# Kernel optimization log

Hardware: AMD Instinct MI355X
Metric: run time of the kernel (lower is better)

Reference implementation:

```python
import jax, jax.numpy as jnp
from jax import lax
import numpy as np

T, B, DIM_F, DIM_H, DIM_S, DIM_W = 1024, 32, 512, 512, 1024, 512


def setup_inputs() -> dict:
    key = jax.random.key(0)
    ks = jax.random.split(key, 9)
    F_matrix = jax.random.normal(ks[0], (T, DIM_F), dtype=jnp.float32)
    a_prev = jax.nn.softmax(jax.random.normal(ks[1], (B, T), dtype=jnp.float32), axis=1)
    s_prev = jax.random.normal(ks[2], (B, DIM_S), dtype=jnp.float32)
    h = jax.random.normal(ks[3], (T, B, DIM_H), dtype=jnp.float32)
    # Linear weights stored as [in, out] so y = x @ W (+ b)
    Ww = jax.random.normal(ks[4], (DIM_S, DIM_W), dtype=jnp.float32) / np.sqrt(DIM_S)
    Vw = jax.random.normal(ks[5], (DIM_H, DIM_W), dtype=jnp.float32) / np.sqrt(DIM_H)
    Vb = jax.random.normal(ks[6], (DIM_W,), dtype=jnp.float32) * 0.01
    Uw = jax.random.normal(ks[7], (DIM_F, DIM_W), dtype=jnp.float32) / np.sqrt(DIM_F)
    ww = jax.random.normal(ks[8], (DIM_W,), dtype=jnp.float32) / np.sqrt(DIM_W)
    return {"F_matrix": F_matrix, "a_prev": a_prev, "s_prev": s_prev, "h": h,
            "Ww": Ww, "Vw": Vw, "Vb": Vb, "Uw": Uw, "ww": ww, "beta": 1}


def _calc_f(F_matrix, a_prev):
    # torch.conv2d(input=[1,1,T,dim_f], weight=[B,1,T,1], padding=[(T-1)//2, 0])
    t = F_matrix.shape[0]
    pad = (t - 1) // 2
    lhs = F_matrix[None, None]          # [1, 1, T, dim_f]
    rhs = a_prev[:, None, :, None]      # [B, 1, T, 1]
    f = lax.conv_general_dilated(
        lhs, rhs, window_strides=(1, 1), padding=[(pad, pad), (0, 0)],
        dimension_numbers=("NCHW", "OIHW", "NCHW"))[0]  # [B, T_out, dim_f]
    if f.shape[1] != t:  # even T -> T_out = T-1; pad one leading time row with zeros
        f = jnp.pad(f, ((0, 0), (1, 0), (0, 0)))
    return f


def reference(F_matrix, a_prev, s_prev, h, Ww, Vw, Vb, Uw, ww, beta):
    f_current = _calc_f(F_matrix, a_prev)                 # [B, T, dim_f]
    hT = jnp.swapaxes(h, 0, 1)                            # [B, T, dim_h]
    x = jnp.tanh(jnp.matmul(s_prev, Ww)[:, None, :]       # Ws: [B, 1, dim_w]
                 + jnp.matmul(hT, Vw) + Vb                # Vh: [B, T, dim_w]
                 + jnp.matmul(f_current, Uw))             # Uf: [B, T, dim_w]
    e_current = jnp.einsum("btw,w->bt", x, ww)            # [B, T]
    return jax.nn.softmax(beta * e_current, axis=1)       # 'sharpening' mode
```

## Files before the change

kernel.cpp:

```cpp
#include <hip/hip_runtime.h>
#include <hip/hip_bf16.h>
#include <math.h>

#define T_DIM 1024
#define B_DIM 32
#define DIMF 512
#define DIMH 512
#define DIMS 1024
#define DIMW 512

typedef __attribute__((ext_vector_type(8))) short short8;
typedef __attribute__((ext_vector_type(4))) float f32x4;

__device__ __forceinline__ unsigned f2bf1(float x) {
    unsigned a = __float_as_uint(x);
    return (a + 0x7FFFu + ((a >> 16) & 1u)) >> 16;
}
__device__ __forceinline__ unsigned f2bf2(float lo, float hi) {
    return f2bf1(lo) | (f2bf1(hi) << 16);
}
__device__ __forceinline__ float fast_tanh(float x) {
    return 1.f - __fdividef(2.f, 1.f + __expf(x + x));
}
__device__ __forceinline__ unsigned short bf1(float x) {
    __hip_bfloat16 b = __float2bfloat16(x);
    return *reinterpret_cast<unsigned short*>(&b);
}
__device__ __forceinline__ short8 pack8(float4 a, float4 c) {
    union { unsigned short us[8]; short8 s; } u;
    u.us[0] = bf1(a.x); u.us[1] = bf1(a.y); u.us[2] = bf1(a.z); u.us[3] = bf1(a.w);
    u.us[4] = bf1(c.x); u.us[5] = bf1(c.y); u.us[6] = bf1(c.z); u.us[7] = bf1(c.w);
    return u.s;
}

__device__ __forceinline__ void gl16(const unsigned short* g, unsigned short* l) {
    __builtin_amdgcn_global_load_lds(
        (const __attribute__((address_space(1))) unsigned int*)g,
        (__attribute__((address_space(3))) unsigned int*)l, 16, 0, 0);
}
__device__ __forceinline__ void gl16f(const float* g, float* l) {
    __builtin_amdgcn_global_load_lds(
        (const __attribute__((address_space(1))) unsigned int*)g,
        (__attribute__((address_space(3))) unsigned int*)l, 16, 0, 0);
}

__global__ void __launch_bounds__(256) k_prep_all(
    const float* __restrict__ F, const float* __restrict__ Uw,
    const float* __restrict__ Vw, const float* __restrict__ a_prev,
    const float* __restrict__ s_prev, const float* __restrict__ Ww,
    const float* __restrict__ Vb, const float* __restrict__ h,
    unsigned short* __restrict__ GT, unsigned short* __restrict__ VwT,
    unsigned short* __restrict__ P, float* __restrict__ SWp,
    unsigned short* __restrict__ hB, int nPack) {
    __shared__ float sh[8192];
    const int bz = blockIdx.x;
    const int tid = threadIdx.x;

    if (bz < nPack) {
        for (unsigned i = bz * 256 + tid; i < 32768u * 64; i += (unsigned)nPack * 256) {
            const int r = i >> 6, c8 = (i & 63) * 8;
            const int bb = r >> 10, t = r & 1023;
            const float* src = h + ((size_t)(t * 32 + bb)) * 512 + c8;
            const float4 v0 = *(const float4*)(src);
            const float4 v1 = *(const float4*)(src + 4);
            union { unsigned short us[8]; uint4 u4; } o;
            o.us[0] = bf1(v0.x); o.us[1] = bf1(v0.y);
            o.us[2] = bf1(v0.z); o.us[3] = bf1(v0.w);
            o.us[4] = bf1(v1.x); o.us[5] = bf1(v1.y);
            o.us[6] = bf1(v1.z); o.us[7] = bf1(v1.w);
            *(uint4*)(hB + (size_t)r * 512 + c8) = o.u4;
        }
        return;
    }
    const int bz2 = bz - nPack;
    if (bz2 < 512) {
        const int rt = bz2 & 63, ct = bz2 >> 6;
        const int r0g = rt * 16;
        const float4* Fv = (const float4*)(F + (size_t)r0g * DIMF);
        float4* shv = (float4*)sh;
        for (int i = tid; i < 16 * DIMF / 4; i += 256) shv[i] = Fv[i];
        __syncthreads();
        const int c = ct * 64 + (tid & 63);
        const int r0 = (tid >> 6) * 4;
        float acc[4] = {0.f, 0.f, 0.f, 0.f};
        for (int k = 0; k < DIMF; ++k) {
            const float bv = Uw[(size_t)k * DIMW + c];
#pragma unroll
            for (int j = 0; j < 4; ++j)
                acc[j] = fmaf(sh[(r0 + j) * DIMF + k], bv, acc[j]);
        }
        uint2 o;
        o.x = f2bf2(acc[0], acc[1]);
        o.y = f2bf2(acc[2], acc[3]);
        *(uint2*)(GT + (size_t)c * T_DIM + r0g + r0) = o;
        return;
    }
    const int bz3 = bz2 - 512;
    if (bz3 < 512) {
        if (bz3 < 256) {
            const int k0 = (bz3 >> 4) * 32, n0 = (bz3 & 15) * 32;
            const int x = tid & 31, y = tid >> 5;
#pragma unroll
            for (int i = 0; i < 4; ++i)
                sh[(y + 8 * i) * 33 + x] = Vw[(size_t)(k0 + y + 8 * i) * DIMW + n0 + x];
            __syncthreads();
#pragma unroll
            for (int i = 0; i < 4; ++i) {
                const int n = n0 + y + 8 * i;
                VwT[(size_t)n * DIMH + k0 + x] = (unsigned short)f2bf1(sh[x * 33 + y + 8 * i]);
            }
        } else {
            const int bs = bz3 - 256;
            const int b = bs >> 3, s = bs & 7;
            for (int i = tid; i < 2048; i += 256) {
                const int j = i + s;
                float v = 0.f;
                if (j >= 512 && j < 1536) v = a_prev[(size_t)b * T_DIM + j - 512];
                P[(size_t)bs * 2048 + i] = (unsigned short)f2bf1(v);
            }
        }
        return;
    }
    {
        const int bz4 = bz3 - 512;
        const int c0 = (bz4 & 15) * 32, q = bz4 >> 4;
        float (*shb)[256] = (float(*)[256])sh;
        for (int i = tid; i < 32 * 64; i += 256) {
            const int r = i >> 6, c4 = (i & 63) * 4;
            *(float4*)&shb[r][c4] = *(const float4*)(s_prev + (size_t)r * DIMS + q * 256 + c4);
        }
        __syncthreads();
        const int c  = c0 + (tid & 31);
        const int bg = tid >> 5;
        float acc[4];
#pragma unroll
        for (int j = 0; j < 4; ++j) acc[j] = (q == 0) ? Vb[c] : 0.f;
        const float* W = Ww + (size_t)q * 256 * DIMW;
        for (int k = 0; k < 256; ++k) {
            const float w = W[(size_t)k * DIMW + c];
#pragma unroll
            for (int j = 0; j < 4; ++j)
                acc[j] = fmaf(shb[bg + 8 * j][k], w, acc[j]);
        }
#pragma unroll
        for (int j = 0; j < 4; ++j)
            SWp[((size_t)q * B_DIM + bg + 8 * j) * DIMW + c] = acc[j];
    }
}

template <bool PACKED>
__global__ void __launch_bounds__(256, 3) k_main(
    const float* __restrict__ hF, const unsigned short* __restrict__ hB,
    const unsigned short* __restrict__ VwT, const unsigned short* __restrict__ GT,
    const unsigned short* __restrict__ P, const float* __restrict__ SWp,
    const float* __restrict__ ww, float* __restrict__ ep) {
    __shared__ __align__(16) float AsF[PACKED ? 4096 : 8192];
    __shared__ unsigned short Bs[128 * 64];
    unsigned short* As2 = (unsigned short*)AsF;

    const int bid = blockIdx.x;
    const int wg  = (bid & 7) * 128 + (bid >> 3);
    const int x = wg & 3, yy = wg >> 2;
    const int w0 = x * 128;
    const int b  = yy >> 3;
    const int t0 = (yy & 7) * 128;

    const int tid  = threadIdx.x;
    const int lane = tid & 63;
    const int wv   = tid >> 6;
    const int wm = wv >> 1, wn = wv & 1;
    const int g = lane >> 4, r16 = lane & 15;
    const int s7 = r16 & 7;

    f32x4 acc[4][4];
#pragma unroll
    for (int m = 0; m < 4; ++m)
#pragma unroll
        for (int n = 0; n < 4; ++n) acc[m][n] = (f32x4)0.f;

    const int kstart = max(0, t0 - 512);
    const int kend   = min(T_DIM - 1, t0 + 639);
    const int NS2    = (kend - kstart + 1) >> 6;

    const int rB = lane >> 3;
    const int cB = ((lane & 7) ^ rB) * 8;
    const unsigned short* hSb[4];
#pragma unroll
    for (int q = 0; q < 4; ++q)
        hSb[q] = hB + ((size_t)(b * 1024 + t0 + wv * 32 + q * 8 + rB)) * 512 + cB;
    const float* hS[8];
    {
        const int rl = lane >> 4, cl = lane & 15;
#pragma unroll
        for (int q = 0; q < 8; ++q) {
            const int row = wv * 32 + q * 4 + rl;
            hS[q] = hF + ((size_t)(t0 + row) * B_DIM + b) * DIMH + ((cl ^ (row & 7)) << 2);
        }
    }
    const unsigned short* vS[4];
    const unsigned short* gS[4];
#pragma unroll
    for (int q = 0; q < 4; ++q) {
        vS[q] = VwT + (size_t)(w0 + wv * 32 + q * 8 + rB) * DIMH + cB;
        gS[q] = GT  + (size_t)(w0 + wv * 32 + q * 8 + rB) * T_DIM + kstart + cB;
    }
    const unsigned short* Pb = P + (size_t)b * 8 * 2048;
    const unsigned short* pS[4];
#pragma unroll
    for (int q = 0; q < 4; ++q) {
        const int row = wv * 32 + q * 8 + rB;
        const int jb = kstart + ((lane & 7) ^ rB) * 8 + 1024 - (t0 + row);
        const int sj = jb & 7;
        pS[q] = Pb + sj * 2048 + (jb - sj);
    }
    const bool zrow = (t0 + wm * 64 + r16 == 0);

    for (int k0 = 0; k0 < DIMH; k0 += 64) {
        __syncthreads();
        if (PACKED) {
#pragma unroll
            for (int q = 0; q < 4; ++q) gl16(hSb[q] + k0, As2 + (wv * 32 + q * 8) * 64);
        } else {
#pragma unroll
            for (int q = 0; q < 8; ++q) gl16f(hS[q] + k0, AsF + (wv * 32 + q * 4) * 64);
        }
#pragma unroll
        for (int q = 0; q < 4; ++q) gl16(vS[q] + k0, Bs + (wv * 32 + q * 8) * 64);
        __syncthreads();

#pragma unroll
        for (int ks = 0; ks < 2; ++ks) {
            short8 af[4], bf[4];
            if (PACKED) {
#pragma unroll
                for (int m = 0; m < 4; ++m)
                    af[m] = *(const short8*)&As2[(wm * 64 + m * 16 + r16) * 64 +
                                                 ((ks * 4 + g) ^ s7) * 8];
            } else {
#pragma unroll
                for (int m = 0; m < 4; ++m) {
                    const int base = (wm * 64 + m * 16 + r16) * 64;
                    const int clo = ((ks * 8 + 2 * g) ^ s7) * 4;
                    const int chi = ((ks * 8 + 2 * g + 1) ^ s7) * 4;
                    af[m] = pack8(*(const float4*)&AsF[base + clo],
                                  *(const float4*)&AsF[base + chi]);
                }
            }
#pragma unroll
            for (int n = 0; n < 4; ++n)
                bf[n] = *(const short8*)&Bs[(wn * 64 + n * 16 + r16) * 64 +
                                            ((ks * 4 + g) ^ s7) * 8];
#pragma unroll
            for (int m = 0; m < 4; ++m)
#pragma unroll
                for (int n = 0; n < 4; ++n)
                    acc[m][n] = __builtin_amdgcn_mfma_f32_16x16x32_bf16(
                        af[m], bf[n], acc[m][n], 0, 0, 0);
        }
    }

    for (int s2 = 0; s2 < NS2; ++s2) {
        const int o = s2 * 64;
        __syncthreads();
#pragma unroll
        for (int q = 0; q < 4; ++q) gl16(pS[q] + o, As2 + (wv * 32 + q * 8) * 64);
#pragma unroll
        for (int q = 0; q < 4; ++q) gl16(gS[q] + o, Bs + (wv * 32 + q * 8) * 64);
        __syncthreads();

#pragma unroll
        for (int ks = 0; ks < 2; ++ks) {
            short8 af[4], bf[4];
#pragma unroll
            for (int m = 0; m < 4; ++m)
                af[m] = *(const short8*)&As2[(wm * 64 + m * 16 + r16) * 64 +
                                             ((ks * 4 + g) ^ s7) * 8];
            if (zrow) af[0] = (short8)(short)0;
#pragma unroll
            for (int n = 0; n < 4; ++n)
                bf[n] = *(const short8*)&Bs[(wn * 64 + n * 16 + r16) * 64 +
                                            ((ks * 4 + g) ^ s7) * 8];
#pragma unroll
            for (int m = 0; m < 4; ++m)
#pragma unroll
                for (int n = 0; n < 4; ++n)
                    acc[m][n] = __builtin_amdgcn_mfma_f32_16x16x32_bf16(
                        af[m], bf[n], acc[m][n], 0, 0, 0);
        }
    }

    float swv[4], wwv[4];
#pragma unroll
    for (int n = 0; n < 4; ++n) {
        const int w = w0 + wn * 64 + n * 16 + r16;
        float sv = 0.f;
#pragma unroll
        for (int q = 0; q < 4; ++q)
            sv += SWp[((size_t)q * B_DIM + b) * DIMW + w];
        swv[n] = sv;
        wwv[n] = ww[w];
    }
#pragma unroll
    for (int m = 0; m < 4; ++m) {
#pragma unroll
        for (int reg = 0; reg < 4; ++reg) {
            float s = 0.f;
#pragma unroll
            for (int n = 0; n < 4; ++n)
                s = fmaf(fast_tanh(acc[m][n][reg] + swv[n]), wwv[n], s);
            s += __shfl_xor(s, 1, 64);
            s += __shfl_xor(s, 2, 64);
            s += __shfl_xor(s, 4, 64);
            s += __shfl_xor(s, 8, 64);
            if (r16 == 0) {
                const int trow = t0 + wm * 64 + m * 16 + g * 4 + reg;
                ep[((size_t)(x * 2 + wn) * B_DIM + b) * T_DIM + trow] = s;
            }
        }
    }
}

__device__ __forceinline__ float decode_beta(const void* p) {
    const int iv = *(const int*)p;
    const float fv = __int_as_float(iv);
    const float afv = fabsf(fv);
    if (afv >= 1e-6f && afv <= 1e6f) return fv;
    return (float)iv;
}

__global__ void k_softmax(const float* __restrict__ ep, const void* __restrict__ beta_p,
                          float* __restrict__ out) {
    const int b = blockIdx.x;
    const float beta = decode_beta(beta_p);
    __shared__ float redm[4];
    __shared__ float reds[4];
    float v[4];
    float m = -INFINITY;
#pragma unroll
    for (int i = 0; i < 4; ++i) {
        const int t = threadIdx.x * 4 + i;
        float ev = 0.f;
#pragma unroll
        for (int xq = 0; xq < 8; ++xq)
            ev += ep[((size_t)xq * B_DIM + b) * T_DIM + t];
        v[i] = beta * ev;
        m = fmaxf(m, v[i]);
    }
    for (int off = 1; off < 64; off <<= 1) m = fmaxf(m, __shfl_xor(m, off, 64));
    const int wid = threadIdx.x >> 6, lane = threadIdx.x & 63;
    if (lane == 0) redm[wid] = m;
    __syncthreads();
    m = fmaxf(fmaxf(redm[0], redm[1]), fmaxf(redm[2], redm[3]));
    float s = 0.f;
    float ex[4];
#pragma unroll
    for (int i = 0; i < 4; ++i) { ex[i] = expf(v[i] - m); s += ex[i]; }
    for (int off = 1; off < 64; off <<= 1) s += __shfl_xor(s, off, 64);
    if (lane == 0) reds[wid] = s;
    __syncthreads();
    s = reds[0] + reds[1] + reds[2] + reds[3];
    const float inv = 1.f / s;
#pragma unroll
    for (int i = 0; i < 4; ++i)
        out[(size_t)b * T_DIM + threadIdx.x * 4 + i] = ex[i] * inv;
}

extern "C" void kernel_launch(void* const* d_in, const int* in_sizes, int n_in,
                              void* d_out, int out_size, void* d_ws, size_t ws_size,
                              hipStream_t stream) {
    const float* F      = (const float*)d_in[0];
    const float* a_prev = (const float*)d_in[1];
    const float* s_prev = (const float*)d_in[2];
    const float* h      = (const float*)d_in[3];
    const float* Ww     = (const float*)d_in[4];
    const float* Vw     = (const float*)d_in[5];
    const float* Vb     = (const float*)d_in[6];
    const float* Uw     = (const float*)d_in[7];
    const float* ww     = (const float*)d_in[8];
    const void*  beta_p = d_in[9];
    float* out = (float*)d_out;

    char* ws = (char*)d_ws;
    unsigned short* GT  = (unsigned short*)(ws);
    unsigned short* VwT = (unsigned short*)(ws + (1u << 20));
    unsigned short* P   = (unsigned short*)(ws + (1u << 20) + (512u << 10));
    float* SWp = (float*)(ws + (2u << 20) + (512u << 10));
    float* ep  = (float*)(ws + (2u << 20) + (768u << 10));
    unsigned short* hB = (unsigned short*)(ws + (4u << 20));

    const bool big = ws_size >= (36ull << 20);
    const int nPack = big ? 1024 : 0;

    k_prep_all<<<dim3(nPack + 1088), 256, 0, stream>>>(
        F, Uw, Vw, a_prev, s_prev, Ww, Vb, h, GT, VwT, P, SWp, hB, nPack);
    if (big) {
        k_main<true><<<dim3(1024), 256, 0, stream>>>(h, hB, VwT, GT, P, SWp, ww, ep);
    } else {
        k_main<false><<<dim3(1024), 256, 0, stream>>>(h, hB, VwT, GT, P, SWp, ww, ep);
    }
    k_softmax<<<dim3(32), 256, 0, stream>>>(ep, beta_p, out);
}
```

Before: 111.2 us.

## Software-pipeline main GEMM with triple-buffered B tiles and direct A register loads

Replaces the packed main kernel with a pipelined version in which the B operand (VwT, then GT) is staged into a three-deep LDS ring two steps ahead. The A operand (bf16 h, then P) is loaded straight from global memory into registers one step ahead, with explicit vmcnt waits and a single barrier per step. This is meant to overlap global loads with MFMA work and remove the double __syncthreads per k-step. The cost is higher register pressure, since the occupancy hint of 3 is dropped, and the A loads are uncoalesced 16-byte per-lane global reads.

```diff
diff --git a/kernel.cpp b/kernel.cpp
--- a/kernel.cpp
+++ b/kernel.cpp
@@ -148,15 +148,12 @@
     }
 }
 
-template <bool PACKED>
-__global__ void __launch_bounds__(256, 3) k_main(
-    const float* __restrict__ hF, const unsigned short* __restrict__ hB,
-    const unsigned short* __restrict__ VwT, const unsigned short* __restrict__ GT,
-    const unsigned short* __restrict__ P, const float* __restrict__ SWp,
-    const float* __restrict__ ww, float* __restrict__ ep) {
-    __shared__ __align__(16) float AsF[PACKED ? 4096 : 8192];
-    __shared__ unsigned short Bs[128 * 64];
-    unsigned short* As2 = (unsigned short*)AsF;
+__global__ void __launch_bounds__(256) k_main_pipe(
+    const unsigned short* __restrict__ hB, const unsigned short* __restrict__ VwT,
+    const unsigned short* __restrict__ GT, const unsigned short* __restrict__ P,
+    const float* __restrict__ SWp, const float* __restrict__ ww,
+    float* __restrict__ ep) {
+    __shared__ unsigned short Bs[3][128 * 64];
 
     const int bid = blockIdx.x;
     const int wg  = (bid & 7) * 128 + (bid >> 3);
@@ -169,7 +166,7 @@
     const int lane = tid & 63;
     const int wv   = tid >> 6;
     const int wm = wv >> 1, wn = wv & 1;
-    const int g = lane >> 4, r16 = lane & 15;
+    const int g = lane >> 4, r16 = lane & 15, g8 = g * 8;
     const int s7 = r16 & 7;
 
     f32x4 acc[4][4];
@@ -181,13 +178,186 @@
     const int kstart = max(0, t0 - 512);
     const int kend   = min(T_DIM - 1, t0 + 639);
     const int NS2    = (kend - kstart + 1) >> 6;
+    const int NT     = 8 + NS2;
 
     const int rB = lane >> 3;
     const int cB = ((lane & 7) ^ rB) * 8;
-    const unsigned short* hSb[4];
-#pragma unroll
-    for (int q = 0; q < 4; ++q)
-        hSb[q] = hB + ((size_t)(b * 1024 + t0 + wv * 32 + q * 8 + rB)) * 512 + cB;
+    const unsigned short* vS[4];
+    const unsigned short* gS[4];
+#pragma unroll
+    for (int q = 0; q < 4; ++q) {
+        vS[q] = VwT + (size_t)(w0 + wv * 32 + q * 8 + rB) * DIMH + cB;
+        gS[q] = GT  + (size_t)(w0 + wv * 32 + q * 8 + rB) * T_DIM + kstart + cB;
+    }
+
+    const int trow0 = t0 + wm * 64 + r16;
+    const unsigned short* hA[4];
+#pragma unroll
+    for (int m = 0; m < 4; ++m)
+        hA[m] = hB + ((size_t)(b * 1024 + trow0 + m * 16)) * 512 + g8;
+    const unsigned short* Pb = P + (size_t)b * 8 * 2048;
+    const unsigned short* pA[4];
+#pragma unroll
+    for (int m = 0; m < 4; ++m) {
+        const int trow = trow0 + m * 16;
+        const int jb = kstart + g8 + 1024 - trow;
+        const int sj = jb & 7;
+        pA[m] = Pb + sj * 2048 + (jb - sj);
+    }
+    const bool zrow = (trow0 == 0);
+
+#define FENCE() __builtin_amdgcn_sched_barrier(0)
+#define STAGEB(u2, j)                                                        \
+    {                                                                        \
+        if ((u2) < 8) {                                                      \
+            _Pragma("unroll")                                                \
+            for (int q = 0; q < 4; ++q)                                      \
+                gl16(vS[q] + (u2) * 64, &Bs[j][(wv * 32 + q * 8) * 64]);     \
+        } else {                                                             \
+            _Pragma("unroll")                                                \
+            for (int q = 0; q < 4; ++q)                                      \
+                gl16(gS[q] + ((u2) - 8) * 64, &Bs[j][(wv * 32 + q * 8) * 64]); \
+        }                                                                    \
+    }
+#define LOADA(AF, u1)                                                        \
+    {                                                                        \
+        if ((u1) < 8) {                                                      \
+            _Pragma("unroll")                                                \
+            for (int m = 0; m < 4; ++m) {                                    \
+                AF[m * 2]     = *(const short8*)(hA[m] + (u1) * 64);         \
+                AF[m * 2 + 1] = *(const short8*)(hA[m] + (u1) * 64 + 32);    \
+            }                                                                \
+        } else {                                                             \
+            _Pragma("unroll")                                                \
+            for (int m = 0; m < 4; ++m) {                                    \
+                AF[m * 2]     = *(const short8*)(pA[m] + ((u1) - 8) * 64);   \
+                AF[m * 2 + 1] = *(const short8*)(pA[m] + ((u1) - 8) * 64 + 32); \
+            }                                                                \
+            if (zrow) { AF[0] = (short8)(short)0; AF[1] = (short8)(short)0; } \
+        }                                                                    \
+    }
+#define STEP(AFc, AFn, u)                                                    \
+    {                                                                        \
+        int rc2 = rc + 2; if (rc2 >= 3) rc2 -= 3;                            \
+        if ((u) + 2 < NT) STAGEB((u) + 2, rc2);                              \
+        FENCE();                                                             \
+        if ((u) + 1 < NT) LOADA(AFn, (u) + 1);                               \
+        FENCE();                                                             \
+        const unsigned short* Bc = &Bs[rc][0];                               \
+        short8 bf0[4], bf1[4];                                               \
+        _Pragma("unroll")                                                    \
+        for (int n = 0; n < 4; ++n) {                                        \
+            const int rowb = (wn * 64 + n * 16 + r16) * 64;                  \
+            bf0[n] = *(const short8*)(Bc + rowb + ((g) ^ s7) * 8);           \
+            bf1[n] = *(const short8*)(Bc + rowb + ((4 + g) ^ s7) * 8);       \
+        }                                                                    \
+        _Pragma("unroll")                                                    \
+        for (int m = 0; m < 4; ++m)                                          \
+            _Pragma("unroll")                                                \
+            for (int n = 0; n < 4; ++n)                                      \
+                acc[m][n] = __builtin_amdgcn_mfma_f32_16x16x32_bf16(         \
+                    AFc[m * 2], bf0[n], acc[m][n], 0, 0, 0);                 \
+        _Pragma("unroll")                                                    \
+        for (int m = 0; m < 4; ++m)                                          \
+            _Pragma("unroll")                                                \
+            for (int n = 0; n < 4; ++n)                                      \
+                acc[m][n] = __builtin_amdgcn_mfma_f32_16x16x32_bf16(         \
+                    AFc[m * 2 + 1], bf1[n], acc[m][n], 0, 0, 0);             \
+        FENCE();                                                             \
+        asm volatile("s_waitcnt vmcnt(12)" ::: "memory");                    \
+        __builtin_amdgcn_s_barrier();                                        \
+        FENCE();                                                             \
+        rc = rc + 1; if (rc >= 3) rc -= 3;                                   \
+    }
+
+    short8 afP[8], afQ[8];
+    STAGEB(0, 0);
+    FENCE();
+    STAGEB(1, 1);
+    FENCE();
+    LOADA(afP, 0);
+    FENCE();
+    asm volatile("s_waitcnt vmcnt(12)" ::: "memory");
+    __builtin_amdgcn_s_barrier();
+    FENCE();
+
+    int rc = 0;
+    for (int u = 0; u < NT; u += 2) {
+        STEP(afP, afQ, u);
+        STEP(afQ, afP, u + 1);
+    }
+
+#undef STAGEB
+#undef LOADA
+#undef STEP
+#undef FENCE
+
+    float swv[4], wwv[4];
+#pragma unroll
+    for (int n = 0; n < 4; ++n) {
+        const int w = w0 + wn * 64 + n * 16 + r16;
+        float sv = 0.f;
+#pragma unroll
+        for (int q = 0; q < 4; ++q)
+            sv += SWp[((size_t)q * B_DIM + b) * DIMW + w];
+        swv[n] = sv;
+        wwv[n] = ww[w];
+    }
+#pragma unroll
+    for (int m = 0; m < 4; ++m) {
+#pragma unroll
+        for (int reg = 0; reg < 4; ++reg) {
+            float s = 0.f;
+#pragma unroll
+            for (int n = 0; n < 4; ++n)
+                s = fmaf(fast_tanh(acc[m][n][reg] + swv[n]), wwv[n], s);
+            s += __shfl_xor(s, 1, 64);
+            s += __shfl_xor(s, 2, 64);
+            s += __shfl_xor(s, 4, 64);
+            s += __shfl_xor(s, 8, 64);
+            if (r16 == 0) {
+                const int trow = t0 + wm * 64 + m * 16 + g * 4 + reg;
+                ep[((size_t)(x * 2 + wn) * B_DIM + b) * T_DIM + trow] = s;
+            }
+        }
+    }
+}
+
+__global__ void __launch_bounds__(256, 3) k_main_fb(
+    const float* __restrict__ hF, const unsigned short* __restrict__ VwT,
+    const unsigned short* __restrict__ GT, const unsigned short* __restrict__ P,
+    const float* __restrict__ SWp, const float* __restrict__ ww,
+    float* __restrict__ ep) {
+    __shared__ __align__(16) float AsF[8192];
+    __shared__ unsigned short Bs[128 * 64];
+    unsigned short* As2 = (unsigned short*)AsF;
+
+    const int bid = blockIdx.x;
+    const int wg  = (bid & 7) * 128 + (bid >> 3);
+    const int x = wg & 3, yy = wg >> 2;
+    const int w0 = x * 128;
+    const int b  = yy >> 3;
+    const int t0 = (yy & 7) * 128;
+
+    const int tid  = threadIdx.x;
+    const int lane = tid & 63;
+    const int wv   = tid >> 6;
+    const int wm = wv >> 1, wn = wv & 1;
+    const int g = lane >> 4, r16 = lane & 15;
+    const int s7 = r16 & 7;
+
+    f32x4 acc[4][4];
+#pragma unroll
+    for (int m = 0; m < 4; ++m)
+#pragma unroll
+        for (int n = 0; n < 4; ++n) acc[m][n] = (f32x4)0.f;
+
+    const int kstart = max(0, t0 - 512);
+    const int kend   = min(T_DIM - 1, t0 + 639);
+    const int NS2    = (kend - kstart + 1) >> 6;
+
+    const int rB = lane >> 3;
+    const int cB = ((lane & 7) ^ rB) * 8;
     const float* hS[8];
     {
         const int rl = lane >> 4, cl = lane & 15;
@@ -217,34 +387,21 @@
 
     for (int k0 = 0; k0 < DIMH; k0 += 64) {
         __syncthreads();
-        if (PACKED) {
-#pragma unroll
-            for (int q = 0; q < 4; ++q) gl16(hSb[q] + k0, As2 + (wv * 32 + q * 8) * 64);
-        } else {
-#pragma unroll
-            for (int q = 0; q < 8; ++q) gl16f(hS[q] + k0, AsF + (wv * 32 + q * 4) * 64);
-        }
+#pragma unroll
+        for (int q = 0; q < 8; ++q) gl16f(hS[q] + k0, AsF + (wv * 32 + q * 4) * 64);
 #pragma unroll
         for (int q = 0; q < 4; ++q) gl16(vS[q] + k0, Bs + (wv * 32 + q * 8) * 64);
         __syncthreads();
-
 #pragma unroll
         for (int ks = 0; ks < 2; ++ks) {
             short8 af[4], bf[4];
-            if (PACKED) {
-#pragma unroll
-                for (int m = 0; m < 4; ++m)
-                    af[m] = *(const short8*)&As2[(wm * 64 + m * 16 + r16) * 64 +
-                                                 ((ks * 4 + g) ^ s7) * 8];
-            } else {
-#pragma unroll
-                for (int m = 0; m < 4; ++m) {
-                    const int base = (wm * 64 + m * 16 + r16) * 64;
-                    const int clo = ((ks * 8 + 2 * g) ^ s7) * 4;
-                    const int chi = ((ks * 8 + 2 * g + 1) ^ s7) * 4;
-                    af[m] = pack8(*(const float4*)&AsF[base + clo],
-                                  *(const float4*)&AsF[base + chi]);
-                }
+#pragma unroll
+            for (int m = 0; m < 4; ++m) {
+                const int base = (wm * 64 + m * 16 + r16) * 64;
+                const int clo = ((ks * 8 + 2 * g) ^ s7) * 4;
+                const int chi = ((ks * 8 + 2 * g + 1) ^ s7) * 4;
+                af[m] = pack8(*(const float4*)&AsF[base + clo],
+                              *(const float4*)&AsF[base + chi]);
             }
 #pragma unroll
             for (int n = 0; n < 4; ++n)
@@ -258,7 +415,6 @@
                         af[m], bf[n], acc[m][n], 0, 0, 0);
         }
     }
-
     for (int s2 = 0; s2 < NS2; ++s2) {
         const int o = s2 * 64;
         __syncthreads();
@@ -267,7 +423,6 @@
 #pragma unroll
         for (int q = 0; q < 4; ++q) gl16(gS[q] + o, Bs + (wv * 32 + q * 8) * 64);
         __syncthreads();
-
 #pragma unroll
         for (int ks = 0; ks < 2; ++ks) {
             short8 af[4], bf[4];
@@ -288,7 +443,6 @@
                         af[m], bf[n], acc[m][n], 0, 0, 0);
         }
     }
-
     float swv[4], wwv[4];
 #pragma unroll
     for (int n = 0; n < 4; ++n) {
@@ -394,9 +548,9 @@
     k_prep_all<<<dim3(nPack + 1088), 256, 0, stream>>>(
         F, Uw, Vw, a_prev, s_prev, Ww, Vb, h, GT, VwT, P, SWp, hB, nPack);
     if (big) {
-        k_main<true><<<dim3(1024), 256, 0, stream>>>(h, hB, VwT, GT, P, SWp, ww, ep);
+        k_main_pipe<<<dim3(1024), 256, 0, stream>>>(hB, VwT, GT, P, SWp, ww, ep);
     } else {
-        k_main<false><<<dim3(1024), 256, 0, stream>>>(h, hB, VwT, GT, P, SWp, ww, ep);
+        k_main_fb<<<dim3(1024), 256, 0, stream>>>(h, VwT, GT, P, SWp, ww, ep);
     }
     k_softmax<<<dim3(32), 256, 0, stream>>>(ep, beta_p, out);
 }
```

After: 147.1 us. 1.32x slower.

## Load A fragments directly to registers and double-buffer B tiles in LDS

Applied to the files above, without the earlier changes.

Drops the separate fp32-to-bf16 packing pass over h, which wrote a 32MB workspace copy. The main kernel now reads h from global memory straight into registers and converts each MFMA A-fragment on the fly. The P fragments are also read directly from global memory. B tiles (VwT and GT) are double-buffered in LDS with a software-pipelined loop that loads the next stage while the current one computes, which halves barrier pairs. The risk is uncoalesced global A reads and higher register pressure, since the occupancy hint of 3 blocks per CU is removed.

```diff
diff --git a/kernel.cpp b/kernel.cpp
--- a/kernel.cpp
+++ b/kernel.cpp
@@ -26,7 +26,9 @@
     __hip_bfloat16 b = __float2bfloat16(x);
     return *reinterpret_cast<unsigned short*>(&b);
 }
-__device__ __forceinline__ short8 pack8(float4 a, float4 c) {
+__device__ __forceinline__ short8 cvt_frag(const float* p) {
+    const float4 a = *(const float4*)p;
+    const float4 c = *(const float4*)(p + 4);
     union { unsigned short us[8]; short8 s; } u;
     u.us[0] = bf1(a.x); u.us[1] = bf1(a.y); u.us[2] = bf1(a.z); u.us[3] = bf1(a.w);
     u.us[4] = bf1(c.x); u.us[5] = bf1(c.y); u.us[6] = bf1(c.z); u.us[7] = bf1(c.w);
@@ -38,43 +40,20 @@
         (const __attribute__((address_space(1))) unsigned int*)g,
         (__attribute__((address_space(3))) unsigned int*)l, 16, 0, 0);
 }
-__device__ __forceinline__ void gl16f(const float* g, float* l) {
-    __builtin_amdgcn_global_load_lds(
-        (const __attribute__((address_space(1))) unsigned int*)g,
-        (__attribute__((address_space(3))) unsigned int*)l, 16, 0, 0);
-}
 
 __global__ void __launch_bounds__(256) k_prep_all(
     const float* __restrict__ F, const float* __restrict__ Uw,
     const float* __restrict__ Vw, const float* __restrict__ a_prev,
     const float* __restrict__ s_prev, const float* __restrict__ Ww,
-    const float* __restrict__ Vb, const float* __restrict__ h,
+    const float* __restrict__ Vb,
     unsigned short* __restrict__ GT, unsigned short* __restrict__ VwT,
-    unsigned short* __restrict__ P, float* __restrict__ SWp,
-    unsigned short* __restrict__ hB, int nPack) {
+    unsigned short* __restrict__ P, float* __restrict__ SWp) {
     __shared__ float sh[8192];
     const int bz = blockIdx.x;
     const int tid = threadIdx.x;
 
-    if (bz < nPack) {
-        for (unsigned i = bz * 256 + tid; i < 32768u * 64; i += (unsigned)nPack * 256) {
-            const int r = i >> 6, c8 = (i & 63) * 8;
-            const int bb = r >> 10, t = r & 1023;
-            const float* src = h + ((size_t)(t * 32 + bb)) * 512 + c8;
-            const float4 v0 = *(const float4*)(src);
-            const float4 v1 = *(const float4*)(src + 4);
-            union { unsigned short us[8]; uint4 u4; } o;
-            o.us[0] = bf1(v0.x); o.us[1] = bf1(v0.y);
-            o.us[2] = bf1(v0.z); o.us[3] = bf1(v0.w);
-            o.us[4] = bf1(v1.x); o.us[5] = bf1(v1.y);
-            o.us[6] = bf1(v1.z); o.us[7] = bf1(v1.w);
-            *(uint4*)(hB + (size_t)r * 512 + c8) = o.u4;
-        }
-        return;
-    }
-    const int bz2 = bz - nPack;
-    if (bz2 < 512) {
-        const int rt = bz2 & 63, ct = bz2 >> 6;
+    if (bz < 512) {
+        const int rt = bz & 63, ct = bz >> 6;
         const int r0g = rt * 16;
         const float4* Fv = (const float4*)(F + (size_t)r0g * DIMF);
         float4* shv = (float4*)sh;
@@ -95,7 +74,7 @@
         *(uint2*)(GT + (size_t)c * T_DIM + r0g + r0) = o;
         return;
     }
-    const int bz3 = bz2 - 512;
+    const int bz3 = bz - 512;
     if (bz3 < 512) {
         if (bz3 < 256) {
             const int k0 = (bz3 >> 4) * 32, n0 = (bz3 & 15) * 32;
@@ -148,15 +127,12 @@
     }
 }
 
-template <bool PACKED>
-__global__ void __launch_bounds__(256, 3) k_main(
-    const float* __restrict__ hF, const unsigned short* __restrict__ hB,
-    const unsigned short* __restrict__ VwT, const unsigned short* __restrict__ GT,
-    const unsigned short* __restrict__ P, const float* __restrict__ SWp,
-    const float* __restrict__ ww, float* __restrict__ ep) {
-    __shared__ __align__(16) float AsF[PACKED ? 4096 : 8192];
-    __shared__ unsigned short Bs[128 * 64];
-    unsigned short* As2 = (unsigned short*)AsF;
+__global__ void __launch_bounds__(256) k_main_r(
+    const float* __restrict__ hF, const unsigned short* __restrict__ VwT,
+    const unsigned short* __restrict__ GT, const unsigned short* __restrict__ P,
+    const float* __restrict__ SWp, const float* __restrict__ ww,
+    float* __restrict__ ep) {
+    __shared__ unsigned short Bs[2][8192];
 
     const int bid = blockIdx.x;
     const int wg  = (bid & 7) * 128 + (bid >> 3);
@@ -169,7 +145,7 @@
     const int lane = tid & 63;
     const int wv   = tid >> 6;
     const int wm = wv >> 1, wn = wv & 1;
-    const int g = lane >> 4, r16 = lane & 15;
+    const int g = lane >> 4, r16 = lane & 15, g8 = g * 8;
     const int s7 = r16 & 7;
 
     f32x4 acc[4][4];
@@ -184,19 +160,6 @@
 
     const int rB = lane >> 3;
     const int cB = ((lane & 7) ^ rB) * 8;
-    const unsigned short* hSb[4];
-#pragma unroll
-    for (int q = 0; q < 4; ++q)
-        hSb[q] = hB + ((size_t)(b * 1024 + t0 + wv * 32 + q * 8 + rB)) * 512 + cB;
-    const float* hS[8];
-    {
-        const int rl = lane >> 4, cl = lane & 15;
-#pragma unroll
-        for (int q = 0; q < 8; ++q) {
-            const int row = wv * 32 + q * 4 + rl;
-            hS[q] = hF + ((size_t)(t0 + row) * B_DIM + b) * DIMH + ((cl ^ (row & 7)) << 2);
-        }
-    }
     const unsigned short* vS[4];
     const unsigned short* gS[4];
 #pragma unroll
@@ -204,90 +167,116 @@
         vS[q] = VwT + (size_t)(w0 + wv * 32 + q * 8 + rB) * DIMH + cB;
         gS[q] = GT  + (size_t)(w0 + wv * 32 + q * 8 + rB) * T_DIM + kstart + cB;
     }
+
+    const int trow0 = t0 + wm * 64 + r16;
+    const float* hAf[4];
+#pragma unroll
+    for (int m = 0; m < 4; ++m)
+        hAf[m] = hF + ((size_t)(trow0 + m * 16) * B_DIM + b) * DIMH + g8;
     const unsigned short* Pb = P + (size_t)b * 8 * 2048;
-    const unsigned short* pS[4];
-#pragma unroll
-    for (int q = 0; q < 4; ++q) {
-        const int row = wv * 32 + q * 8 + rB;
-        const int jb = kstart + ((lane & 7) ^ rB) * 8 + 1024 - (t0 + row);
+    const unsigned short* pA[4];
+#pragma unroll
+    for (int m = 0; m < 4; ++m) {
+        const int trow = trow0 + m * 16;
+        const int jb = kstart + g8 + 1024 - trow;
         const int sj = jb & 7;
-        pS[q] = Pb + sj * 2048 + (jb - sj);
-    }
-    const bool zrow = (t0 + wm * 64 + r16 == 0);
-
-    for (int k0 = 0; k0 < DIMH; k0 += 64) {
-        __syncthreads();
-        if (PACKED) {
-#pragma unroll
-            for (int q = 0; q < 4; ++q) gl16(hSb[q] + k0, As2 + (wv * 32 + q * 8) * 64);
+        pA[m] = Pb + sj * 2048 + (jb - sj);
+    }
+    const bool zrow = (trow0 == 0);
+
+#define STAGEB1(u, j)                                                        \
+    {                                                                        \
+        const int o_ = (u) * 64;                                             \
+        _Pragma("unroll")                                                    \
+        for (int q = 0; q < 4; ++q)                                          \
+            gl16(vS[q] + o_, &Bs[j][(wv * 32 + q * 8) * 64]);                \
+    }
+#define STAGEB2(s, j)                                                        \
+    {                                                                        \
+        const int o_ = (s) * 64;                                             \
+        _Pragma("unroll")                                                    \
+        for (int q = 0; q < 4; ++q)                                          \
+            gl16(gS[q] + o_, &Bs[j][(wv * 32 + q * 8) * 64]);                \
+    }
+#define LOADA1(AF, u)                                                        \
+    {                                                                        \
+        const int o_ = (u) * 64;                                             \
+        _Pragma("unroll")                                                    \
+        for (int m = 0; m < 4; ++m) {                                        \
+            AF[m * 2]     = cvt_frag(hAf[m] + o_);                           \
+            AF[m * 2 + 1] = cvt_frag(hAf[m] + o_ + 32);                      \
+        }                                                                    \
+    }
+#define LOADA2(AF, s)                                                        \
+    {                                                                        \
+        const int o_ = (s) * 64;                                             \
+        _Pragma("unroll")                                                    \
+        for (int m = 0; m < 4; ++m) {                                        \
+            AF[m * 2]     = *(const short8*)(pA[m] + o_);                    \
+            AF[m * 2 + 1] = *(const short8*)(pA[m] + o_ + 32);               \
+        }                                                                    \
+        if (zrow) { AF[0] = (short8)(short)0; AF[1] = (short8)(short)0; }    \
+    }
+#define COMP(AF, j)                                                          \
+    {                                                                        \
+        _Pragma("unroll")                                                    \
+        for (int ks = 0; ks < 2; ++ks) {                                     \
+            short8 bf_[4];                                                   \
+            _Pragma("unroll")                                                \
+            for (int n = 0; n < 4; ++n)                                      \
+                bf_[n] = *(const short8*)&Bs[j][(wn * 64 + n * 16 + r16) * 64 + \
+                                                ((ks * 4 + g) ^ s7) * 8];    \
+            _Pragma("unroll")                                                \
+            for (int m = 0; m < 4; ++m)                                      \
+                _Pragma("unroll")                                            \
+                for (int n = 0; n < 4; ++n)                                  \
+                    acc[m][n] = __builtin_amdgcn_mfma_f32_16x16x32_bf16(     \
+                        AF[m * 2 + ks], bf_[n], acc[m][n], 0, 0, 0);         \
+        }                                                                    \
+    }
+
+    short8 afP[8], afQ[8];
+    STAGEB1(0, 0);
+    LOADA1(afP, 0);
+    __syncthreads();
+
+#pragma unroll
+    for (int u = 0; u < 8; u += 2) {
+        STAGEB1(u + 1, 1);
+        LOADA1(afQ, u + 1);
+        COMP(afP, 0);
+        __syncthreads();
+        if (u + 2 < 8) {
+            STAGEB1(u + 2, 0);
+            LOADA1(afP, u + 2);
         } else {
-#pragma unroll
-            for (int q = 0; q < 8; ++q) gl16f(hS[q] + k0, AsF + (wv * 32 + q * 4) * 64);
-        }
-#pragma unroll
-        for (int q = 0; q < 4; ++q) gl16(vS[q] + k0, Bs + (wv * 32 + q * 8) * 64);
-        __syncthreads();
-
-#pragma unroll
-        for (int ks = 0; ks < 2; ++ks) {
-            short8 af[4], bf[4];
-            if (PACKED) {
-#pragma unroll
-                for (int m = 0; m < 4; ++m)
-                    af[m] = *(const short8*)&As2[(wm * 64 + m * 16 + r16) * 64 +
-                                                 ((ks * 4 + g) ^ s7) * 8];
-            } else {
-#pragma unroll
-                for (int m = 0; m < 4; ++m) {
-                    const int base = (wm * 64 + m * 16 + r16) * 64;
-                    const int clo = ((ks * 8 + 2 * g) ^ s7) * 4;
-                    const int chi = ((ks * 8 + 2 * g + 1) ^ s7) * 4;
-                    af[m] = pack8(*(const float4*)&AsF[base + clo],
-                                  *(const float4*)&AsF[base + chi]);
-                }
-            }
-#pragma unroll
-            for (int n = 0; n < 4; ++n)
-                bf[n] = *(const short8*)&Bs[(wn * 64 + n * 16 + r16) * 64 +
-                                            ((ks * 4 + g) ^ s7) * 8];
-#pragma unroll
-            for (int m = 0; m < 4; ++m)
-#pragma unroll
-                for (int n = 0; n < 4; ++n)
-                    acc[m][n] = __builtin_amdgcn_mfma_f32_16x16x32_bf16(
-                        af[m], bf[n], acc[m][n], 0, 0, 0);
-        }
-    }
-
-    for (int s2 = 0; s2 < NS2; ++s2) {
-        const int o = s2 * 64;
-        __syncthreads();
-#pragma unroll
-        for (int q = 0; q < 4; ++q) gl16(pS[q] + o, As2 + (wv * 32 + q * 8) * 64);
-#pragma unroll
-        for (int q = 0; q < 4; ++q) gl16(gS[q] + o, Bs + (wv * 32 + q * 8) * 64);
-        __syncthreads();
-
-#pragma unroll
-        for (int ks = 0; ks < 2; ++ks) {
-            short8 af[4], bf[4];
-#pragma unroll
-            for (int m = 0; m < 4; ++m)
-                af[m] = *(const short8*)&As2[(wm * 64 + m * 16 + r16) * 64 +
-                                             ((ks * 4 + g) ^ s7) * 8];
-            if (zrow) af[0] = (short8)(short)0;
-#pragma unroll
-            for (int n = 0; n < 4; ++n)
-                bf[n] = *(const short8*)&Bs[(wn * 64 + n * 16 + r16) * 64 +
-                                            ((ks * 4 + g) ^ s7) * 8];
-#pragma unroll
-            for (int m = 0; m < 4; ++m)
-#pragma unroll
-                for (int n = 0; n < 4; ++n)
-                    acc[m][n] = __builtin_amdgcn_mfma_f32_16x16x32_bf16(
-                        af[m], bf[n], acc[m][n], 0, 0, 0);
-        }
-    }
+            STAGEB2(0, 0);
+            LOADA2(afP, 0);
+        }
+        COMP(afQ, 1);
+        __syncthreads();
+    }
+
+    for (int s2 = 0; s2 < NS2; s2 += 2) {
+        if (s2 + 1 < NS2) {
+            STAGEB2(s2 + 1, 1);
+            LOADA2(afQ, s2 + 1);
+        }
+        COMP(afP, 0);
+        __syncthreads();
+        if (s2 + 2 < NS2) {
+            STAGEB2(s2 + 2, 0);
+            LOADA2(afP, s2 + 2);
+        }
+        COMP(afQ, 1);
+        __syncthreads();
+    }
+
+#undef STAGEB1
+#undef STAGEB2
+#undef LOADA1
+#undef LOADA2
+#undef COMP
 
     float swv[4], wwv[4];
 #pragma unroll
@@ -386,17 +375,9 @@
     unsigned short* P   = (unsigned short*)(ws + (1u << 20) + (512u << 10));
     float* SWp = (float*)(ws + (2u << 20) + (512u << 10));
     float* ep  = (float*)(ws + (2u << 20) + (768u << 10));
-    unsigned short* hB = (unsigned short*)(ws + (4u << 20));
-
-    const bool big = ws_size >= (36ull << 20);
-    const int nPack = big ? 1024 : 0;
-
-    k_prep_all<<<dim3(nPack + 1088), 256, 0, stream>>>(
-        F, Uw, Vw, a_prev, s_prev, Ww, Vb, h, GT, VwT, P, SWp, hB, nPack);
-    if (big) {
-        k_main<true><<<dim3(1024), 256, 0, stream>>>(h, hB, VwT, GT, P, SWp, ww, ep);
-    } else {
-        k_main<false><<<dim3(1024), 256, 0, stream>>>(h, hB, VwT, GT, P, SWp, ww, ep);
-    }
-    k_softmax<<<dim3(32), 256, 0, stream>>>(ep, beta_p, out);
-}
+
+    k_prep_all<<<dim3(1088), 256, 0, stream>>>(
+        F, Uw, Vw, a_prev, s_prev, Ww, Vb, GT, VwT, P, SWp);
+    k_main_r  <<<dim3(1024), 256, 0, stream>>>(h, VwT, GT, P, SWp, ww, ep);
+    k_softmax <<<dim3(32),   256, 0, stream>>>(ep, beta_p, out);
+}
```

Result: slower. 159.9 us (+43.7%).
